# Performance work log

Measured on AMD Instinct MI355X. Metric: run time of the kernel, lower is better.

## Reference

```python
import jax, jax.numpy as jnp
import numpy as np

STEP = 16
LEAK = 32
KSIZE = STEP + LEAK          # 48
PAD = 32                     # ceil((48+16)/2)
THETA = 25.6                 # dense(0.05) * synapses(512) * input_channel(1)
FODEP = 48                   # = kernel_size
BIAS = 0.5
OUT_CH = 1


def setup_inputs() -> dict:
    key = jax.random.key(0)
    k1, k2 = jax.random.split(key, 2)
    input_spikes = (jax.random.uniform(k1, (16, 1, 512, 512)) < 0.05).astype(jnp.float32)
    # weight ~ Exponential(rate=1/w_init) with w_init=0.5, clipped to [0,1]
    u = jax.random.uniform(k2, (1024, 512), minval=1e-6, maxval=1.0)
    weight = jnp.clip(-0.5 * jnp.log(u), 0.0, 1.0)
    return {"input_spikes": input_spikes, "weight": weight}


def _winner_takes_all(potentials):
    # potentials: [B, C, N, T] -> iterate over time with sequential depression state
    p = jnp.transpose(potentials, (3, 1, 0, 2))  # [T, C, B, N]
    T, C, B, N = p.shape

    def step(dep, p_t):
        # dep: [C, B, N] depression counters (integer-valued floats)
        wins = []
        for c in range(C):
            pot = p_t[c] * (dep[c] == 0)                      # mask depressed neurons
            widx = jnp.argmax(pot, axis=-1)                   # [B]
            wval = jnp.take_along_axis(pot, widx[:, None], axis=-1)[:, 0]
            spike = (wval > THETA).astype(pot.dtype)          # [B]
            win = jax.nn.one_hot(widx, N, dtype=pot.dtype) * spike[:, None]  # [B, N]
            # torch: scatter_add(-spike*fodep at winner) then += spike*fodep broadcast
            dep = dep.at[c].add(spike[:, None] * FODEP - win * FODEP)
            # torch: depression += winners[t, c] * fodep (all channels)
            dep = dep + win[None] * FODEP
            wins.append(win)
        dep = jnp.clip(dep - 1.0, 0.0, FODEP - 1.0)
        return dep, jnp.stack(wins, 0)                        # [C, B, N]

    dep0 = jnp.zeros((C, B, N), p.dtype)
    _, winners = jax.lax.scan(step, dep0, p)                  # winners: [T, C, B, N]
    return jnp.transpose(winners, (2, 1, 3, 0))               # [B, C, N, T]


def _forward(input_spikes, weight):
    B, Ci, S, T = input_spikes.shape
    x = input_spikes.reshape(B, Ci * S, T)
    # StepFireLeak.get_weight_kernel
    t = jnp.arange(KSIZE, dtype=weight.dtype)                 # [K]
    t_spike = t / STEP                                        # [K]
    t_leak = -(t - weight[..., None] * STEP) / LEAK + weight[..., None]  # [O, I, K]
    kernel = jnp.maximum(0.0, jnp.minimum(t_spike, t_leak))[..., ::-1]   # [O, I, K] flipped
    pot = jax.lax.conv_general_dilated(
        x, kernel, window_strides=(1,), padding=[(PAD, PAD)],
        dimension_numbers=('NCH', 'OIH', 'NCH'))              # [B, O*N, T']
    N = weight.shape[0] // OUT_CH
    pot = pot.reshape(B, OUT_CH, N, -1) + BIAS * THETA        # labels=None branch
    return _winner_takes_all(pot)


def reference(input_spikes, weight):
    return _forward(input_spikes, weight)
```

## Files before the change

kernel.cpp:

```cpp
#include <hip/hip_runtime.h>
#include <stdint.h>


#define NB 16
#define NI 512
#define NT 512
#define NO 1024
#define TOUT 529
#define SCAP 96
#define OTILE 4
#define NCELL 562
#define DUST 561u
#define THETA_F 25.6f
#define BIAS_T 12.8f

__global__ __launch_bounds__(256) void k_spikes(const float* __restrict__ x,
                                                unsigned short* __restrict__ slist,
                                                unsigned int* __restrict__ spkw,
                                                unsigned int* __restrict__ counts) {
    __shared__ unsigned short sls[4][SCAP];
    int wq = threadIdx.x >> 6, lane = threadIdx.x & 63;
    int row = blockIdx.x * 4 + wq;
    const float* xr = x + (size_t)row * NT;
    for (int j = lane; j < SCAP; j += 64) sls[wq][j] = 0xFFFFu;
    int base = 0;
    for (int kk = 0; kk < 8; ++kk) {
        int t = kk * 64 + lane;
        bool pred = xr[t] > 0.5f;
        unsigned long long mask = __ballot(pred);
        int pre = __popcll(mask & ((1ull << lane) - 1ull));
        int pos = base + pre;
        if (pred && pos < SCAP) sls[wq][pos] = (unsigned short)t;
        base += __popcll(mask);
    }
    __syncthreads();
    if (lane < SCAP / 2) {
        unsigned v = (unsigned)sls[wq][2 * lane] | ((unsigned)sls[wq][2 * lane + 1] << 16);
        ((unsigned int*)(slist + (size_t)row * SCAP))[lane] = v;
    }
    if (lane < 32)
        spkw[(size_t)row * 32 + lane] = (unsigned)sls[wq][lane] | ((unsigned)sls[wq][lane + 32] << 16);
    if (lane == 0) counts[row] = (unsigned)min(base, SCAP);
}

__global__ __launch_bounds__(256) void k_hist(const float* __restrict__ x,
                                              float* __restrict__ hg) {
    int b = blockIdx.y, seg = blockIdx.z;
    int t = blockIdx.x * 256 + threadIdx.x;
    const float* xb = x + (size_t)b * NI * NT + (size_t)seg * 64 * NT + t;
    float s0 = 0.f, s1 = 0.f, s2 = 0.f, s3 = 0.f;
    for (int i = 0; i < 64; i += 4) {
        s0 += xb[(size_t)i * NT];       s1 += xb[(size_t)(i + 1) * NT];
        s2 += xb[(size_t)(i + 2) * NT]; s3 += xb[(size_t)(i + 3) * NT];
    }
    unsafeAtomicAdd(&hg[b * NT + t], (s0 + s1) + (s2 + s3));
}

__global__ __launch_bounds__(256) void k_taps(const float* __restrict__ weight,
                                              float4* __restrict__ tap) {
    int p = blockIdx.x * 256 + threadIdx.x;
    int o = p >> 9, i = p & 511;
    float w = weight[o * NI + i];
    float b15 = 1.5f * w;
    float vA1 = 0.f, vA2 = 0.f, vB1 = 0.f, vB2 = 0.f;
    int posA = 2000, posB = 2000, state = 0;
    float Km1 = 0.f, Km2 = 0.f;
    for (int tau = 0; tau <= 49; ++tau) {
        float K = 0.f;
        if (tau <= 47) {
            float f = (float)tau * 0.0625f;
            float g = b15 - (float)tau * 0.03125f;
            K = fmaxf(0.f, fminf(f, g));
        }
        float d = (K - Km1) - (Km1 - Km2);
        if (tau == 1) d -= 0.0625f;
        if (d != 0.f) {
            if (state == 0)      { posA = tau; vA1 = d; state = 1; }
            else if (state == 1) { if (tau == posA + 1) { vA2 = d; state = 2; }
                                   else { posB = tau; vB1 = d; state = 3; } }
            else if (state == 2) { posB = tau; vB1 = d; state = 3; }
            else if (state == 3) { if (tau == posB + 1) { vB2 = d; state = 4; } }
        }
        Km2 = Km1; Km1 = K;
    }
    size_t base = 2 * ((size_t)o * NI + i);
    tap[base]     = make_float4(vA1, vA2, __int_as_float(posA), 0.f);
    tap[base + 1] = make_float4(vB1, vB2, __int_as_float(posB), 0.f);
}

#define PROC(TP, WV, CNT, IDX)                                                        \
    {                                                                                 \
        const int p = __float_as_int((TP).z);                                         \
        {                                                                             \
            unsigned e = min((unsigned)((int)((WV) & 0xFFFFu) + p), DUST);            \
            float2* cell = (float2*)(accw + e * 4 + ramp2);                           \
            float2 v = *cell; v.x += (TP).x; v.y += (TP).y; *cell = v;                \
        }                                                                             \
        if ((CNT) > 32u) {                                                            \
            unsigned e = min((unsigned)((int)((WV) >> 16) + p), DUST);                \
            float2* cell = (float2*)(accw + e * 4 + ramp2);                           \
            float2 v = *cell; v.x += (TP).x; v.y += (TP).y; *cell = v;                \
        }                                                                             \
        if ((CNT) > 64u) {                                                            \
            const unsigned short* sr = slist + (size_t)(b * NI + (IDX)) * SCAP;       \
            for (int kk = 64 + k; kk < (int)(CNT); kk += 32) {                        \
                unsigned e = min((unsigned)((int)sr[kk] + p), DUST);                  \
                float2* cell = (float2*)(accw + e * 4 + ramp2);                       \
                float2 v = *cell; v.x += (TP).x; v.y += (TP).y; *cell = v;            \
            }                                                                         \
        }                                                                             \
    }

__global__ __launch_bounds__(256, 4) void k_scatter(const unsigned short* __restrict__ slist,
                                                    const unsigned int* __restrict__ spkw,
                                                    const unsigned int* __restrict__ counts,
                                                    const float4* __restrict__ tap,
                                                    const float* __restrict__ hg,
                                                    float* __restrict__ pot) {
    __shared__ float4 acc[OTILE * NCELL];
    __shared__ double pub[512];
    const int o0 = blockIdx.x * OTILE;
    const int b  = blockIdx.y;
    const int tid = threadIdx.x;
    const int w = tid >> 6, lane = tid & 63;
    const int k = lane >> 1, ramp = lane & 1, ramp2 = ramp * 2;

    for (int idx = tid; idx < OTILE * NCELL; idx += 256) acc[idx] = make_float4(0.f, 0.f, 0.f, 0.f);
    __syncthreads();

    float* accw = (float*)(acc + w * NCELL);
    const unsigned int* wrow = spkw + (size_t)(b * NI) * 32 + k;
    const float4* trow = tap + 2 * (size_t)(o0 + w) * NI + ramp;
    const uint4* crow = (const uint4*)(counts + b * NI);

    float4 ntA = trow[0], ntB = trow[2], ntC = trow[4], ntD = trow[6];
    unsigned nwA = wrow[0], nwB = wrow[32], nwC = wrow[64], nwD = wrow[96];
    uint4 ncc = crow[0];

    const int NIQ = NI / 4;
    for (int iq = 0; iq < NIQ; ++iq) {
        const float4 tA = ntA, tB = ntB, tC = ntC, tD = ntD;
        const unsigned wA = nwA, wB = nwB, wC = nwC, wD = nwD;
        const uint4 cc = ncc;
        if (iq + 1 < NIQ) {
            const float4* tb = trow + (size_t)(iq + 1) * 8;
            ntA = tb[0]; ntB = tb[2]; ntC = tb[4]; ntD = tb[6];
            const unsigned int* wb = wrow + (size_t)(iq + 1) * 128;
            nwA = wb[0]; nwB = wb[32]; nwC = wb[64]; nwD = wb[96];
            ncc = crow[iq + 1];
        }
        const int i0 = iq * 4;
        PROC(tA, wA, cc.x, i0)
        PROC(tB, wB, cc.y, i0 + 1)
        PROC(tC, wC, cc.z, i0 + 2)
        PROC(tD, wD, cc.w, i0 + 3)
    }
    __syncthreads();

    const int q = lane;
    const float4* rowQ = acc + w * NCELL;
    const float* hb = hg + b * NT;
    double dsv[9];
    double s1d = 0.0, s2d = 0.0;
#pragma unroll
    for (int r = 0; r < 9; ++r) {
        int e = q * 9 + r;
        double d = 0.0;
        if (e < 561) {
            float4 c = rowQ[e];
            d = (double)c.x + (double)c.z;
            if (e >= 1) {
                float4 cm = rowQ[e - 1];
                d += (double)cm.y + (double)cm.w;
                if (e <= 512) d += 0.0625 * (double)hb[e - 1];
            }
        }
        dsv[r] = d; s1d += d; s2d += s1d;
    }
    pub[2 * tid] = s1d; pub[2 * tid + 1] = s2d;
    __syncthreads();
    if (tid < 4) {
        double c1 = 0.0, c2 = 0.0;
        for (int qq = 0; qq < 64; ++qq) {
            int j = (tid << 6) + qq;
            double S1 = pub[2 * j], S2 = pub[2 * j + 1];
            pub[2 * j] = c1; pub[2 * j + 1] = c2;
            c2 += 9.0 * c1 + S2;
            c1 += S1;
        }
    }
    __syncthreads();
    {
        const double C1 = pub[2 * tid], C2 = pub[2 * tid + 1];
        double a1 = 0.0, a2 = 0.0;
        float4* rowW = acc + w * NCELL;
#pragma unroll
        for (int r = 0; r < 9; ++r) {
            a1 += dsv[r]; a2 += a1;
            int e = q * 9 + r;
            if (e < 561) rowW[e].x = (float)(C2 + C1 * (double)(r + 1) + a2);
        }
    }
    __syncthreads();
    for (int oo = 0; oo < OTILE; ++oo)
        for (int t = tid; t < TOUT; t += 256)
            pot[((size_t)(b * NO + o0 + oo)) * TOUT + t] = acc[oo * NCELL + t + 15].x + BIAS_T;
}

__global__ __launch_bounds__(256) void k_argmax(const float* __restrict__ pot,
                                                float* __restrict__ aval,
                                                unsigned short* __restrict__ aidx) {
    __shared__ float sv[4][64];
    __shared__ int   si[4][64];
    int b = blockIdx.y;
    int t0 = blockIdx.x * 64;
    int lane = threadIdx.x & 63, grp = threadIdx.x >> 6;
    int t = t0 + lane;
    bool valid = t < TOUT;
    float best = -1.f; int bidx = 0;
    if (valid) {
        for (int od = 0; od < 256; ++od) {
            int o = grp * 256 + od;
            float v = pot[((size_t)(b * NO + o)) * TOUT + t];
            if (v > best) { best = v; bidx = o; }
        }
    }
    sv[grp][lane] = best; si[grp][lane] = bidx;
    __syncthreads();
    if (grp == 0 && valid) {
#pragma unroll
        for (int g = 1; g < 4; ++g) {
            float v = sv[g][lane];
            if (v > best) { best = v; bidx = si[g][lane]; }
        }
        aval[t * NB + b] = best;
        aidx[t * NB + b] = (unsigned short)bidx;
    }
}

__global__ __launch_bounds__(256) void k_wta(const float* __restrict__ aval,
                                             const unsigned short* __restrict__ aidx,
                                             float* __restrict__ out) {
    __shared__ float lv[TOUT * NB];
    __shared__ unsigned short li[TOUT * NB];
    for (int idx = threadIdx.x; idx < TOUT * NB; idx += 256) { lv[idx] = aval[idx]; li[idx] = aidx[idx]; }
    __syncthreads();
    int b = threadIdx.x;
    if (b < NB) {
        int r = 0;
        for (int t = 0; t < TOUT; ++t) {
            float v = lv[t * NB + b];
            if (r == 0 && v > THETA_F) {
                int n = (int)li[t * NB + b];
                out[((size_t)(b * NO + n)) * TOUT + t] = 1.0f;
                r = 48;
            }
            r = max(r - 1, 0);
        }
    }
}

extern "C" void kernel_launch(void* const* d_in, const int* in_sizes, int n_in,
                              void* d_out, int out_size, void* d_ws, size_t ws_size,
                              hipStream_t stream) {
    const float* x      = (const float*)d_in[0];
    const float* weight = (const float*)d_in[1];
    float* out = (float*)d_out;
    char* ws = (char*)d_ws;
    unsigned short* slist  = (unsigned short*)(ws);
    unsigned int*   spkw   = (unsigned int*)(ws + 1572864);
    unsigned int*   counts = (unsigned int*)(ws + 2621440);
    float4*         tap    = (float4*)(ws + 2654208);
    float*          hg     = (float*)(ws + 19431424);
    float*          aval   = (float*)(ws + 19464192);
    unsigned short* aidx   = (unsigned short*)(ws + 19498048);

    k_spikes<<<2048, 256, 0, stream>>>(x, slist, spkw, counts);
    hipMemsetAsync(hg, 0, NB * NT * sizeof(float), stream);
    k_hist<<<dim3(2, NB, 8), 256, 0, stream>>>(x, hg);
    k_taps<<<2048, 256, 0, stream>>>(weight, tap);
    k_scatter<<<dim3(NO / OTILE, NB), 256, 0, stream>>>(slist, spkw, counts, tap, hg, out);
    k_argmax<<<dim3(9, 16), 256, 0, stream>>>(out, aval, aidx);
    hipMemsetAsync(d_out, 0, (size_t)out_size * sizeof(float), stream);
    k_wta<<<1, 256, 0, stream>>>(aval, aidx, out);
}
```

Before: 503.3 us.

## Fuse preprocessing kernels, split LDS accumulator planes, zero output inside argmax

Merges the spike-list, histogram and tap kernels into one launch, and drops the histogram memset by reducing through shared memory instead of global atomics. The scatter accumulator moves from interleaved float4 cells to four separate float planes, each padded to PLEN, which changes the LDS access pattern and bank behaviour. The output memset is folded into k_argmax, which zeroes the potentials after reading them. Fewer launches and memsets are the target, at the cost of a larger LDS footprint and a k_argmax that writes the whole output.

```diff
diff --git a/kernel.cpp b/kernel.cpp
--- a/kernel.cpp
+++ b/kernel.cpp
@@ -9,83 +9,88 @@
 #define TOUT 529
 #define SCAP 96
 #define OTILE 4
-#define NCELL 562
-#define DUST 561u
+#define PLEN 571
+#define ROWF 2284
+#define DUST 564u
 #define THETA_F 25.6f
 #define BIAS_T 12.8f
 
-__global__ __launch_bounds__(256) void k_spikes(const float* __restrict__ x,
-                                                unsigned short* __restrict__ slist,
-                                                unsigned int* __restrict__ spkw,
-                                                unsigned int* __restrict__ counts) {
-    __shared__ unsigned short sls[4][SCAP];
-    int wq = threadIdx.x >> 6, lane = threadIdx.x & 63;
-    int row = blockIdx.x * 4 + wq;
-    const float* xr = x + (size_t)row * NT;
-    for (int j = lane; j < SCAP; j += 64) sls[wq][j] = 0xFFFFu;
-    int base = 0;
-    for (int kk = 0; kk < 8; ++kk) {
-        int t = kk * 64 + lane;
-        bool pred = xr[t] > 0.5f;
-        unsigned long long mask = __ballot(pred);
-        int pre = __popcll(mask & ((1ull << lane) - 1ull));
-        int pos = base + pre;
-        if (pred && pos < SCAP) sls[wq][pos] = (unsigned short)t;
-        base += __popcll(mask);
-    }
-    __syncthreads();
-    if (lane < SCAP / 2) {
-        unsigned v = (unsigned)sls[wq][2 * lane] | ((unsigned)sls[wq][2 * lane + 1] << 16);
-        ((unsigned int*)(slist + (size_t)row * SCAP))[lane] = v;
-    }
-    if (lane < 32)
-        spkw[(size_t)row * 32 + lane] = (unsigned)sls[wq][lane] | ((unsigned)sls[wq][lane + 32] << 16);
-    if (lane == 0) counts[row] = (unsigned)min(base, SCAP);
-}
-
-__global__ __launch_bounds__(256) void k_hist(const float* __restrict__ x,
-                                              float* __restrict__ hg) {
-    int b = blockIdx.y, seg = blockIdx.z;
-    int t = blockIdx.x * 256 + threadIdx.x;
-    const float* xb = x + (size_t)b * NI * NT + (size_t)seg * 64 * NT + t;
-    float s0 = 0.f, s1 = 0.f, s2 = 0.f, s3 = 0.f;
-    for (int i = 0; i < 64; i += 4) {
-        s0 += xb[(size_t)i * NT];       s1 += xb[(size_t)(i + 1) * NT];
-        s2 += xb[(size_t)(i + 2) * NT]; s3 += xb[(size_t)(i + 3) * NT];
-    }
-    unsafeAtomicAdd(&hg[b * NT + t], (s0 + s1) + (s2 + s3));
-}
-
-__global__ __launch_bounds__(256) void k_taps(const float* __restrict__ weight,
-                                              float4* __restrict__ tap) {
-    int p = blockIdx.x * 256 + threadIdx.x;
-    int o = p >> 9, i = p & 511;
-    float w = weight[o * NI + i];
-    float b15 = 1.5f * w;
-    float vA1 = 0.f, vA2 = 0.f, vB1 = 0.f, vB2 = 0.f;
-    int posA = 2000, posB = 2000, state = 0;
-    float Km1 = 0.f, Km2 = 0.f;
-    for (int tau = 0; tau <= 49; ++tau) {
-        float K = 0.f;
-        if (tau <= 47) {
-            float f = (float)tau * 0.0625f;
-            float g = b15 - (float)tau * 0.03125f;
-            K = fmaxf(0.f, fminf(f, g));
-        }
-        float d = (K - Km1) - (Km1 - Km2);
-        if (tau == 1) d -= 0.0625f;
-        if (d != 0.f) {
-            if (state == 0)      { posA = tau; vA1 = d; state = 1; }
-            else if (state == 1) { if (tau == posA + 1) { vA2 = d; state = 2; }
-                                   else { posB = tau; vB1 = d; state = 3; } }
-            else if (state == 2) { posB = tau; vB1 = d; state = 3; }
-            else if (state == 3) { if (tau == posB + 1) { vB2 = d; state = 4; } }
-        }
-        Km2 = Km1; Km1 = K;
-    }
-    size_t base = 2 * ((size_t)o * NI + i);
-    tap[base]     = make_float4(vA1, vA2, __int_as_float(posA), 0.f);
-    tap[base + 1] = make_float4(vB1, vB2, __int_as_float(posB), 0.f);
+__global__ __launch_bounds__(256) void k_pre(const float* __restrict__ x,
+                                             const float* __restrict__ weight,
+                                             unsigned short* __restrict__ slist,
+                                             unsigned int* __restrict__ spkw,
+                                             unsigned int* __restrict__ counts,
+                                             float* __restrict__ hg,
+                                             float4* __restrict__ tap) {
+    __shared__ __align__(16) char lsd[1024];
+    const int bid = blockIdx.x;
+    const int tid = threadIdx.x;
+    if (bid < 2048) {
+        unsigned short (*sls)[SCAP] = (unsigned short(*)[SCAP])lsd;
+        int wq = tid >> 6, lane = tid & 63;
+        int row = bid * 4 + wq;
+        const float* xr = x + (size_t)row * NT;
+        for (int j = lane; j < SCAP; j += 64) sls[wq][j] = 0xFFFFu;
+        int base = 0;
+        for (int kk = 0; kk < 8; ++kk) {
+            int t = kk * 64 + lane;
+            bool pred = xr[t] > 0.5f;
+            unsigned long long mask = __ballot(pred);
+            int pre = __popcll(mask & ((1ull << lane) - 1ull));
+            int pos = base + pre;
+            if (pred && pos < SCAP) sls[wq][pos] = (unsigned short)t;
+            base += __popcll(mask);
+        }
+        __syncthreads();
+        if (lane < SCAP / 2) {
+            unsigned v = (unsigned)sls[wq][2 * lane] | ((unsigned)sls[wq][2 * lane + 1] << 16);
+            ((unsigned int*)(slist + (size_t)row * SCAP))[lane] = v;
+        }
+        if (lane < 32)
+            spkw[(size_t)row * 32 + lane] = (unsigned)sls[wq][lane] | ((unsigned)sls[wq][lane + 32] << 16);
+        if (lane == 0) counts[row] = (unsigned)min(base, SCAP);
+    } else if (bid < 2176) {
+        float* hs = (float*)lsd;
+        int bid2 = bid - 2048;
+        int b = bid2 >> 3, seg = bid2 & 7;
+        int t = seg * 64 + (tid & 63), isub = tid >> 6;
+        const float* xb = x + (size_t)b * NI * NT + t;
+        float s = 0.f;
+        for (int i = isub * 128; i < isub * 128 + 128; ++i) s += xb[(size_t)i * NT];
+        hs[tid] = s;
+        __syncthreads();
+        if (tid < 64)
+            hg[b * NT + seg * 64 + tid] = (hs[tid] + hs[tid + 64]) + (hs[tid + 128] + hs[tid + 192]);
+    } else {
+        int p = (bid - 2176) * 256 + tid;
+        int o = p >> 9, i = p & 511;
+        float w = weight[o * NI + i];
+        float b15 = 1.5f * w;
+        float vA1 = 0.f, vA2 = 0.f, vB1 = 0.f, vB2 = 0.f;
+        int posA = 2000, posB = 2000, state = 0;
+        float Km1 = 0.f, Km2 = 0.f;
+        for (int tau = 0; tau <= 49; ++tau) {
+            float K = 0.f;
+            if (tau <= 47) {
+                float f = (float)tau * 0.0625f;
+                float g = b15 - (float)tau * 0.03125f;
+                K = fmaxf(0.f, fminf(f, g));
+            }
+            float d = (K - Km1) - (Km1 - Km2);
+            if (tau == 1) d -= 0.0625f;
+            if (d != 0.f) {
+                if (state == 0)      { posA = tau; vA1 = d; state = 1; }
+                else if (state == 1) { if (tau == posA + 1) { vA2 = d; state = 2; }
+                                       else { posB = tau; vB1 = d; state = 3; } }
+                else if (state == 2) { posB = tau; vB1 = d; state = 3; }
+                else if (state == 3) { if (tau == posB + 1) { vB2 = d; state = 4; } }
+            }
+            Km2 = Km1; Km1 = K;
+        }
+        size_t base = 2 * ((size_t)o * NI + i);
+        tap[base]     = make_float4(vA1, vA2, __int_as_float(posA), 0.f);
+        tap[base + 1] = make_float4(vB1, vB2, __int_as_float(posB), 0.f);
+    }
 }
 
 #define PROC(TP, WV, CNT, IDX)                                                        \
@@ -93,20 +98,23 @@
         const int p = __float_as_int((TP).z);                                         \
         {                                                                             \
             unsigned e = min((unsigned)((int)((WV) & 0xFFFFu) + p), DUST);            \
-            float2* cell = (float2*)(accw + e * 4 + ramp2);                           \
-            float2 v = *cell; v.x += (TP).x; v.y += (TP).y; *cell = v;                \
+            float* c = accw + e;                                                      \
+            float a0 = c[0], a1 = c[PLEN];                                            \
+            c[0] = a0 + (TP).x; c[PLEN] = a1 + (TP).y;                                \
         }                                                                             \
         if ((CNT) > 32u) {                                                            \
             unsigned e = min((unsigned)((int)((WV) >> 16) + p), DUST);                \
-            float2* cell = (float2*)(accw + e * 4 + ramp2);                           \
-            float2 v = *cell; v.x += (TP).x; v.y += (TP).y; *cell = v;                \
+            float* c = accw + e;                                                      \
+            float a0 = c[0], a1 = c[PLEN];                                            \
+            c[0] = a0 + (TP).x; c[PLEN] = a1 + (TP).y;                                \
         }                                                                             \
         if ((CNT) > 64u) {                                                            \
             const unsigned short* sr = slist + (size_t)(b * NI + (IDX)) * SCAP;       \
             for (int kk = 64 + k; kk < (int)(CNT); kk += 32) {                        \
                 unsigned e = min((unsigned)((int)sr[kk] + p), DUST);                  \
-                float2* cell = (float2*)(accw + e * 4 + ramp2);                       \
-                float2 v = *cell; v.x += (TP).x; v.y += (TP).y; *cell = v;            \
+                float* c = accw + e;                                                  \
+                float a0 = c[0], a1 = c[PLEN];                                        \
+                c[0] = a0 + (TP).x; c[PLEN] = a1 + (TP).y;                            \
             }                                                                         \
         }                                                                             \
     }
@@ -117,18 +125,19 @@
                                                     const float4* __restrict__ tap,
                                                     const float* __restrict__ hg,
                                                     float* __restrict__ pot) {
-    __shared__ float4 acc[OTILE * NCELL];
+    __shared__ __align__(16) float acc[OTILE * ROWF];
     __shared__ double pub[512];
     const int o0 = blockIdx.x * OTILE;
     const int b  = blockIdx.y;
     const int tid = threadIdx.x;
     const int w = tid >> 6, lane = tid & 63;
-    const int k = lane >> 1, ramp = lane & 1, ramp2 = ramp * 2;
-
-    for (int idx = tid; idx < OTILE * NCELL; idx += 256) acc[idx] = make_float4(0.f, 0.f, 0.f, 0.f);
-    __syncthreads();
-
-    float* accw = (float*)(acc + w * NCELL);
+    const int k = lane >> 1, ramp = lane & 1;
+
+    for (int idx = tid; idx < OTILE * ROWF / 4; idx += 256)
+        ((float4*)acc)[idx] = make_float4(0.f, 0.f, 0.f, 0.f);
+    __syncthreads();
+
+    float* accw = acc + w * ROWF + ramp * (2 * PLEN);
     const unsigned int* wrow = spkw + (size_t)(b * NI) * 32 + k;
     const float4* trow = tap + 2 * (size_t)(o0 + w) * NI + ramp;
     const uint4* crow = (const uint4*)(counts + b * NI);
@@ -158,7 +167,7 @@
     __syncthreads();
 
     const int q = lane;
-    const float4* rowQ = acc + w * NCELL;
+    const float* row = acc + w * ROWF;
     const float* hb = hg + b * NT;
     double dsv[9];
     double s1d = 0.0, s2d = 0.0;
@@ -166,13 +175,11 @@
     for (int r = 0; r < 9; ++r) {
         int e = q * 9 + r;
         double d = 0.0;
-        if (e < 561) {
-            float4 c = rowQ[e];
-            d = (double)c.x + (double)c.z;
+        if (e < PLEN) {
+            d = (double)row[e] + (double)row[2 * PLEN + e];
             if (e >= 1) {
-                float4 cm = rowQ[e - 1];
-                d += (double)cm.y + (double)cm.w;
-                if (e <= 512) d += 0.0625 * (double)hb[e - 1];
+                d += (double)row[PLEN + e - 1] + (double)row[3 * PLEN + e - 1];
+                if (e <= NT) d += 0.0625 * (double)hb[e - 1];
             }
         }
         dsv[r] = d; s1d += d; s2d += s1d;
@@ -193,21 +200,23 @@
     {
         const double C1 = pub[2 * tid], C2 = pub[2 * tid + 1];
         double a1 = 0.0, a2 = 0.0;
-        float4* rowW = acc + w * NCELL;
+        float* rowW = acc + w * ROWF;
+        double av = 0.0;
 #pragma unroll
         for (int r = 0; r < 9; ++r) {
             a1 += dsv[r]; a2 += a1;
             int e = q * 9 + r;
-            if (e < 561) rowW[e].x = (float)(C2 + C1 * (double)(r + 1) + a2);
+            av = C2 + C1 * (double)(r + 1) + a2;
+            if (e < PLEN) rowW[e] = (float)av;
         }
     }
     __syncthreads();
     for (int oo = 0; oo < OTILE; ++oo)
         for (int t = tid; t < TOUT; t += 256)
-            pot[((size_t)(b * NO + o0 + oo)) * TOUT + t] = acc[oo * NCELL + t + 15].x + BIAS_T;
-}
-
-__global__ __launch_bounds__(256) void k_argmax(const float* __restrict__ pot,
+            pot[((size_t)(b * NO + o0 + oo)) * TOUT + t] = acc[oo * ROWF + t + 15] + BIAS_T;
+}
+
+__global__ __launch_bounds__(256) void k_argmax(float* __restrict__ pot,
                                                 float* __restrict__ aval,
                                                 unsigned short* __restrict__ aidx) {
     __shared__ float sv[4][64];
@@ -236,6 +245,11 @@
         aval[t * NB + b] = best;
         aidx[t * NB + b] = (unsigned short)bidx;
     }
+    for (int idx = threadIdx.x; idx < NO * 64; idx += 256) {
+        int o = idx >> 6, tt = idx & 63;
+        int tz = t0 + tt;
+        if (tz < TOUT) pot[((size_t)(b * NO + o)) * TOUT + tz] = 0.f;
+    }
 }
 
 __global__ __launch_bounds__(256) void k_wta(const float* __restrict__ aval,
@@ -275,12 +289,8 @@
     float*          aval   = (float*)(ws + 19464192);
     unsigned short* aidx   = (unsigned short*)(ws + 19498048);
 
-    k_spikes<<<2048, 256, 0, stream>>>(x, slist, spkw, counts);
-    hipMemsetAsync(hg, 0, NB * NT * sizeof(float), stream);
-    k_hist<<<dim3(2, NB, 8), 256, 0, stream>>>(x, hg);
-    k_taps<<<2048, 256, 0, stream>>>(weight, tap);
+    k_pre<<<4224, 256, 0, stream>>>(x, weight, slist, spkw, counts, hg, tap);
     k_scatter<<<dim3(NO / OTILE, NB), 256, 0, stream>>>(slist, spkw, counts, tap, hg, out);
     k_argmax<<<dim3(9, 16), 256, 0, stream>>>(out, aval, aidx);
-    hipMemsetAsync(d_out, 0, (size_t)out_size * sizeof(float), stream);
     k_wta<<<1, 256, 0, stream>>>(aval, aidx, out);
 }
```

Result: slower. 548.2 us (+8.9%).
